# Kernel tuning notes

Hardware: AMD Instinct MI355X
Metric: run time of the kernel (lower is better)

Reference implementation:

```python
import jax, jax.numpy as jnp
import numpy as np

NUM_WIRES = 16
DEPTH = 3
BATCH = 128
DIM = 2 ** NUM_WIRES


def _apply_1q(psi, U, w, n):
    # Apply 2x2 gate U on wire w (wire 0 = most significant bit, PennyLane convention).
    B = psi.shape[0]
    psi = psi.reshape(B, 2 ** w, 2, -1)
    psi = jnp.einsum('ij,bpjq->bpiq', U, psi)
    return psi.reshape(B, -1)


def _apply_cnot(psi, c, t, n):
    # CNOT with control c, target t: flip target amplitudes where control bit is 1.
    B = psi.shape[0]
    a, b = min(c, t), max(c, t)
    psi = psi.reshape(B, 2 ** a, 2, 2 ** (b - a - 1), 2, 2 ** (n - b - 1))
    if c < t:
        psi = psi.at[:, :, 1].set(psi[:, :, 1, :, ::-1, :])
    else:
        psi = psi.at[:, :, :, :, 1].set(psi[:, :, ::-1, :, 1])
    return psi.reshape(B, -1)


def _pauli_z_signs(n):
    # signs[w, i] = +1 if bit w of basis state i is 0, else -1
    idx = np.arange(2 ** n)
    bits = (idx[None, :] >> (n - 1 - np.arange(n))[:, None]) & 1
    return jnp.asarray(1.0 - 2.0 * bits, dtype=jnp.float32)  # (n, 2^n)


def _circuit_features(state, params, n):
    psi = state.astype(jnp.complex64)  # (B, 2^n)
    depth = params.shape[0]
    half = params * 0.5
    for d in range(depth):
        for w in range(n):
            th, ph = half[d, w, 0], half[d, w, 1]
            cth, sth = jnp.cos(th), jnp.sin(th)
            em = jnp.exp(-1j * ph)   # RZ diag phase exp(-i*phi/2)
            ep = jnp.conj(em)
            # fused U = RZ(phi) @ RY(theta)
            U = jnp.stack([jnp.stack([em * cth, -em * sth]),
                           jnp.stack([ep * sth, ep * cth])])
            psi = _apply_1q(psi, U, w, n)
        for w in range(n - 1):
            psi = _apply_cnot(psi, w, w + 1, n)
        psi = _apply_cnot(psi, n - 1, 0, n)
    probs = psi.real ** 2 + psi.imag ** 2          # (B, 2^n)
    return probs @ _pauli_z_signs(n).T              # (B, n) PauliZ expvals


def setup_inputs() -> dict:
    key = jax.random.key(0)
    k1, k2, k3, k4 = jax.random.split(key, 4)
    state = jax.random.normal(k1, (BATCH, DIM), dtype=jnp.float32)
    state = state / jnp.linalg.norm(state, axis=1, keepdims=True)  # valid quantum state
    params = jax.random.normal(k2, (DEPTH, NUM_WIRES, 2), dtype=jnp.float32)
    head_w = jax.random.normal(k3, (1, NUM_WIRES), dtype=jnp.float32) / np.sqrt(NUM_WIRES)
    head_b = jax.random.normal(k4, (1,), dtype=jnp.float32)
    return {"state_batch": state, "params": params, "head_w": head_w, "head_b": head_b}


def reference(state_batch, params, head_w, head_b):
    feats = _circuit_features(state_batch, params, NUM_WIRES)  # (B, num_wires)
    return (feats @ head_w.T + head_b)[:, 0]                   # (B,)
```

## Files before the change

### kernel.cpp

```cpp
#include <hip/hip_runtime.h>
#include <hip/hip_fp16.h>

#define DIMQ 65536
#define BQ 128

typedef float v2f __attribute__((ext_vector_type(2)));

__host__ __device__ constexpr unsigned ring_map(unsigned x) {
  for (int bc = 15; bc >= 1; --bc) x ^= ((x >> bc) & 1u) << (bc - 1);
  x ^= (x & 1u) << 15;
  return x;
}
__host__ __device__ constexpr unsigned ring_unmap(unsigned y) {
  y ^= (y & 1u) << 15;
  for (int bc = 1; bc <= 15; ++bc) y ^= ((y >> bc) & 1u) << (bc - 1);
  return y;
}
__host__ __device__ constexpr unsigned row_of(int b) {
  return (b <= 14) ? ((0xFFFFu << b) & 0xFFFFu) : 0x7FFFu;
}
__host__ __device__ constexpr int popc16(unsigned v) {
  int c = 0; for (int i = 0; i < 16; ++i) c += (v >> i) & 1; return c;
}
static_assert(ring_unmap(ring_map(0x1234u)) == 0x1234u, "inv");
static_assert(ring_map(ring_unmap(0x5A5Au)) == 0x5A5Au, "inv");
__host__ __device__ constexpr bool check_rows() {
  const unsigned xs[4] = {0x1234u, 0x8001u, 0xFFFFu, 0x0F0Fu};
  for (int b = 0; b < 16; ++b)
    for (int i = 0; i < 4; ++i)
      if (((ring_map(xs[i]) >> b) & 1u) != (unsigned)(popc16(xs[i] & row_of(b)) & 1))
        return false;
  return true;
}
static_assert(check_rows(), "row_of = row b of M");
static_assert(ring_unmap(1u << 0)  == 0xC001u, "u0 = e0^e14^e15");
static_assert(ring_unmap(1u << 6)  == 0x0060u, "u6 = e5^e6");
static_assert(ring_unmap(1u << 11) == 0x0C00u, "u11 = e10^e11");
static_assert(ring_unmap(1u << 15) == 0xC000u, "u15 = e14^e15");
static_assert(ring_map(0x0C00u) == 0x0800u, "M(e10^e11)=e11");
static_assert(ring_map(0xC000u) == 0x8000u, "M(e14^e15)=e15");

__host__ __device__ constexpr unsigned loc13(unsigned z16) {
  return (z16 & 0x0FFFu) | (((z16 >> 15) & 1u) << 12);
}
__host__ __device__ constexpr unsigned sw13(unsigned i) { return i ^ ((i >> 5) & 31u); }

struct Tab32u { unsigned v[32]; };
__host__ __device__ constexpr Tab32u make_rx2() {
  Tab32u t{}; for (int r = 0; r < 32; ++r) t.v[r] = (unsigned)r << 11; return t;
}
__host__ __device__ constexpr Tab32u make_swrl() {
  Tab32u t{}; for (int r = 0; r < 32; ++r) t.v[r] = sw13(loc13(ring_map((unsigned)r)));
  return t;
}
__host__ __device__ constexpr Tab32u make_sw2() {
  Tab32u t{}; for (int r = 0; r < 32; ++r) t.v[r] = sw13((unsigned)r << 6);
  return t;
}
__host__ __device__ constexpr Tab32u make_rp3() {
  Tab32u t{}; for (int r = 0; r < 32; ++r) t.v[r] = (unsigned)r << 6; return t;
}
__host__ __device__ constexpr Tab32u make_t4() {
  Tab32u t{};
  for (int r = 0; r < 32; ++r) {
    unsigned r0 = r & 1, r1 = (r >> 1) & 1, r2 = (r >> 2) & 1, r3 = (r >> 3) & 1, r4 = (r >> 4) & 1;
    t.v[r] = (r0 << 10) | ((r0 ^ r1) << 11) | ((r1 ^ r2) << 12) |
             ((r2 ^ r3) << 13) | ((r3 ^ r4) << 14) | (r4 << 15);
  }
  return t;
}
__device__ constexpr Tab32u SWRL = make_swrl();
__device__ constexpr Tab32u SW2  = make_sw2();
__device__ constexpr Tab32u T4   = make_t4();

__host__ __device__ constexpr unsigned clmask(Tab32u t, unsigned row) {
  unsigned m = 0;
  for (int l = 0; l < 32; ++l)
    m |= (unsigned)(popc16(t.v[l] & row) & 1) << l;
  return m;
}
static_assert(clmask(make_t4(), 0xFFFFu) == 0u, "T4 chain has even parity");
static_assert(clmask(make_rx2(), row_of(1)) == 0x96696996u, "thue-morse parity of l");
static_assert((row_of(6) & 63u) == 0u && (row_of(14) & 63u) == 0u, "plain-sum bits");
static_assert((row_of(5) & 63u) == 32u && (row_of(4) & 63u) == 48u, "chain lo");
static_assert((row_of(3) & 63u) == 56u && (row_of(2) & 63u) == 60u, "chain mid");
static_assert((row_of(1) & 63u) == 62u && (row_of(0) & 63u) == 63u, "chain hi");
static_assert((row_of(15) & 63u) == 63u, "bit15 mask");
static_assert((row_of(0) & 31u) == 31u && (row_of(4) & 31u) == 16u, "suffix masks");
static_assert((row_of(5) & 31u) == 0u && (row_of(14) & 31u) == 0u, "rows 5..14 fixed");
static_assert((row_of(15) & 31u) == 31u, "row15 rides u0");
__host__ __device__ constexpr bool check_sufp() {
  for (unsigned r = 0; r < 32; ++r) {
    unsigned u = 0;
    for (int b = 0; b < 5; ++b) {
      unsigned s = 0; for (int j = b; j < 5; ++j) s ^= (r >> j) & 1;
      u |= s << b;
    }
    if ((u ^ (u >> 1)) != r) return false;
  }
  return true;
}
static_assert(check_sufp(), "suffix-parity inverse");

__global__ void k_prep(const float* __restrict__ params, float* __restrict__ uc) {
  int g = threadIdx.x;
  if (g >= 48) return;
  float th = 0.5f * params[g * 2 + 0];
  float ph = 0.5f * params[g * 2 + 1];
  float st, ct, sp, cp;
  __sincosf(th, &st, &ct);
  __sincosf(ph, &sp, &cp);
  float* u = uc + g * 8;
  u[0] = ct; u[1] = st;
  u[2] = cp; u[3] = -sp;
  u[4] = cp * cp - sp * sp;
  u[5] = 2.f * sp * cp;
  u[6] = 0.f; u[7] = 0.f;
}

struct CS { float ct, st; };
__device__ inline CS load_cs(const float* __restrict__ uc, int d, int w) {
  const float* u = uc + (d * 16 + w) * 8;
  return {u[0], u[1]};
}
__device__ inline v2f ldV(const float* __restrict__ uc, int d, int w) {
  const float* u = uc + (d * 16 + w) * 8;
  v2f r; r.x = u[2]; r.y = u[3]; return r;
}
__device__ inline v2f ldR(const float* __restrict__ uc, int d, int w) {
  const float* u = uc + (d * 16 + w) * 8;
  v2f r; r.x = u[4]; r.y = u[5]; return r;
}

__device__ inline v2f splat(float s) { v2f r; r.x = s; r.y = s; return r; }
__device__ inline v2f conjv(v2f a) { v2f r; r.x = a.x; r.y = -a.y; return r; }
__device__ inline v2f dsel(bool c, v2f v) { return c ? conjv(v) : v; }

__device__ inline v2f cmul(v2f c, v2f a) {
  v2f t;
  asm("v_pk_mul_f32 %0, %1, %2 op_sel:[0,0] op_sel_hi:[0,1]"
      : "=v"(t) : "v"(c), "v"(a));
  asm("v_pk_fma_f32 %0, %1, %2, %0 op_sel:[1,1,0] op_sel_hi:[1,0,1] neg_lo:[0,1,0]"
      : "+v"(t) : "v"(c), "v"(a));
  return t;
}
__device__ inline v2f cmulc(v2f c, v2f a) {
  v2f t;
  asm("v_pk_mul_f32 %0, %1, %2 op_sel:[0,0] op_sel_hi:[0,1]"
      : "=v"(t) : "v"(c), "v"(a));
  asm("v_pk_fma_f32 %0, %1, %2, %0 op_sel:[1,1,0] op_sel_hi:[1,0,1] neg_hi:[0,1,0]"
      : "+v"(t) : "v"(c), "v"(a));
  return t;
}

__device__ inline v2f h_to_f2(float bits) {
  __half2 h = __builtin_bit_cast(__half2, bits);
  float2 f = __half22float2(h);
  v2f r; r.x = f.x; r.y = f.y;
  return r;
}
__device__ inline float f2_to_h(v2f v) {
  __half2 h = __float22half2_rn(make_float2(v.x, v.y));
  return __builtin_bit_cast(float, h);
}

template <int MASK>
__device__ inline float lane_xor_f(float v) {
  if constexpr (MASK == 1) {
    return __int_as_float(__builtin_amdgcn_update_dpp(
        0, __float_as_int(v), 0xB1, 0xF, 0xF, true));
  } else if constexpr (MASK == 2) {
    return __int_as_float(__builtin_amdgcn_update_dpp(
        0, __float_as_int(v), 0x4E, 0xF, 0xF, true));
  } else if constexpr (MASK == 3) {
    return __int_as_float(__builtin_amdgcn_update_dpp(
        0, __float_as_int(v), 0x1B, 0xF, 0xF, true));
  } else if constexpr (MASK < 32) {
    return __int_as_float(__builtin_amdgcn_ds_swizzle(
        __float_as_int(v), (MASK << 10) | 0x1F));
  } else {
    return __shfl_xor(v, MASK, 64);
  }
}
template <int MASK>
__device__ inline v2f lane_xor_v(v2f v) {
  v2f r; r.x = lane_xor_f<MASK>(v.x); r.y = lane_xor_f<MASK>(v.y);
  return r;
}

__device__ inline void rmix2(v2f& o0, v2f CT, v2f S0_, v2f A0, v2f B0,
                             v2f& o1, v2f S1_, v2f A1, v2f B1) {
  v2f t0, t1;
  asm("v_pk_mul_f32 %0, %2, %3\n\t"
      "v_pk_mul_f32 %1, %5, %6\n\t"
      "v_pk_fma_f32 %0, %4, %7, %0\n\t"
      "v_pk_fma_f32 %1, %4, %8, %1"
      : "=&v"(t0), "=&v"(t1)
      : "v"(S0_), "v"(B0), "v"(CT), "v"(S1_), "v"(B1), "v"(A0), "v"(A1));
  o0 = t0; o1 = t1;
}

template <int K>
__device__ inline void reg_gate_r(v2f (&a)[32], CS u) {
  const v2f CT = splat(u.ct), SP = splat(u.st), SN = splat(-u.st);
#pragma unroll
  for (int l = 0; l < 32; ++l) {
    if (l & (1 << K)) continue;
    const int p = l | (1 << K);
    const v2f A = a[l], B = a[p];
    rmix2(a[l], CT, SN, A, B,
          a[p],     SP, B, A);
  }
}

template <int MASK>
__device__ inline void lane_gate_r(v2f (&a)[32], CS u, int lane) {
  const bool hi = (lane & MASK) != 0;
  const v2f CT = splat(u.ct), SS = splat(hi ? u.st : -u.st);
#pragma unroll
  for (int l = 0; l < 32; l += 2) {
    v2f p0 = lane_xor_v<MASK>(a[l]);
    v2f p1 = lane_xor_v<MASK>(a[l + 1]);
    rmix2(a[l],     CT, SS, a[l],     p0,
          a[l + 1],     SS, a[l + 1], p1);
  }
}

template <int MASK>
__device__ inline void lane_gate_sr(v2f (&a)[32], CS u, int hi) {
  const v2f CT = splat(u.ct), SS = splat(hi ? u.st : -u.st);
#pragma unroll
  for (int l = 0; l < 32; l += 2) {
    v2f p0 = lane_xor_v<MASK>(a[l]);
    v2f p1 = lane_xor_v<MASK>(a[l + 1]);
    rmix2(a[l],     CT, SS, a[l],     p0,
          a[l + 1],     SS, a[l + 1], p1);
  }
}

template <int PM, unsigned CLM>
__device__ inline void fused_reg_gate_r(v2f (&a)[32], CS u, unsigned xK,
                                        unsigned row) {
  const bool s = (__popc(xK & row) & 1) != 0;
  const v2f CT = splat(u.ct);
  const v2f S0 = splat(s ? u.st : -u.st), NS0 = splat(s ? -u.st : u.st);
  constexpr int LB = PM & (-PM);
#pragma unroll
  for (int l = 0; l < 32; ++l) {
    if (l & LB) continue;
    const int p = l ^ PM;
    const bool cl = (CLM >> l) & 1u;
    const v2f A = a[l], B = a[p];
    rmix2(a[l], CT, cl ? NS0 : S0, A, B,
          a[p],     cl ? S0 : NS0, B, A);
  }
}

template <int LM, unsigned CLM>
__device__ inline void fused_lane_gate_r(v2f (&a)[32], CS u, unsigned xK,
                                         unsigned row) {
  const bool s = (__popc(xK & row) & 1) != 0;
  const v2f CT = splat(u.ct);
  const v2f S0 = splat(s ? u.st : -u.st), NS0 = splat(s ? -u.st : u.st);
#pragma unroll
  for (int l = 0; l < 32; l += 2) {
    v2f p0 = lane_xor_v<LM>(a[l]);
    v2f p1 = lane_xor_v<LM>(a[l + 1]);
    const bool c0 = (CLM >> l) & 1u;
    const bool c1 = (CLM >> (l + 1)) & 1u;
    rmix2(a[l],     CT, c0 ? NS0 : S0, a[l],     p0,
          a[l + 1],     c1 ? NS0 : S0, a[l + 1], p1);
  }
}

template <int LM, int PM, unsigned CLM>
__device__ inline void fused_mixed_gate_r(v2f (&a)[32], CS u, unsigned xK,
                                          unsigned row) {
  const bool s = (__popc(xK & row) & 1) != 0;
  const v2f CT = splat(u.ct);
  const v2f S0 = splat(s ? u.st : -u.st), NS0 = splat(s ? -u.st : u.st);
  constexpr int LB = PM & (-PM);
#pragma unroll
  for (int l = 0; l < 32; ++l) {
    if (l & LB) continue;
    const int p = l ^ PM;
    const bool cl = (CLM >> l) & 1u;
    const bool cp = (CLM >> p) & 1u;
    const v2f A = a[l], B = a[p];
    v2f pa = lane_xor_v<LM>(B);
    v2f pb = lane_xor_v<LM>(A);
    rmix2(a[l], CT, cl ? NS0 : S0, A, pa,
          a[p],     cp ? NS0 : S0, B, pb);
  }
}

__device__ inline void apply_D0(v2f (&a)[32], const float* __restrict__ uc,
                                unsigned xK) {
  v2f c = dsel(xK & 1u, ldV(uc, 0, 15));
#pragma unroll
  for (int j = 1; j <= 10; ++j)
    c = cmul(dsel((xK >> j) & 1u, ldV(uc, 0, 15 - j)), c);
  v2f R[5];
#pragma unroll
  for (int k = 0; k < 5; ++k) {
    c = cmul(ldV(uc, 0, 4 - k), c);
    R[k] = ldR(uc, 0, 4 - k);
  }
  a[0] = cmul(c, a[0]);
#pragma unroll
  for (int i = 1; i < 32; ++i) {
    const int g = i ^ (i >> 1);
    const int k = __builtin_ctz((unsigned)i);
    const bool on = (g >> k) & 1;
    c = on ? cmul(R[k], c) : cmulc(R[k], c);
    a[g] = cmul(c, a[g]);
  }
}

__device__ inline void apply_D1(v2f (&a)[32], const float* __restrict__ uc,
                                unsigned xfull) {
  unsigned q = 0;
#pragma unroll
  for (int b = 0; b < 16; ++b)
    q |= (unsigned)(__popc(xfull & row_of(b)) & 1) << b;
  v2f c = dsel(q & 1u, ldV(uc, 1, 15));
#pragma unroll
  for (int b = 1; b < 16; ++b)
    c = cmul(dsel((q >> b) & 1u, ldV(uc, 1, 15 - b)), c);
  v2f RT[5];
#pragma unroll
  for (int b = 0; b < 5; ++b)
    RT[b] = dsel((q >> b) & 1u, ldR(uc, 1, 15 - b));
  RT[0] = cmul(dsel((q >> 15) & 1u, ldR(uc, 1, 0)), RT[0]);
  a[0] = cmul(c, a[0]);
#pragma unroll
  for (int i = 1; i < 32; ++i) {
    const int u = i ^ (i >> 1);
    const int k = __builtin_ctz((unsigned)i);
    const bool on = (u >> k) & 1;
    c = on ? cmul(RT[k], c) : cmulc(RT[k], c);
    const int r = u ^ (u >> 1);
    a[r] = cmul(c, a[r]);
  }
}

__global__ __launch_bounds__(256, 4)
void k_p1(const float* __restrict__ in, __half2* __restrict__ dstb,
          const float* __restrict__ uc) {
  const int b = blockIdx.x >> 3;
  const unsigned hi = blockIdx.x & 7;
  const unsigned wg = threadIdx.x >> 6;
  const unsigned lane = threadIdx.x & 63;
  const unsigned xK = (hi << 13) | (wg << 11) | (lane << 2);
  const float* src = in + (size_t)b * DIMQ;
  v2f a[32];
#pragma unroll
  for (int c = 0; c < 8; ++c) {
    float4 q = *(const float4*)(src + xK + ((unsigned)c << 8));
    a[c * 4 + 0].x = q.x; a[c * 4 + 0].y = 0.f;
    a[c * 4 + 1].x = q.y; a[c * 4 + 1].y = 0.f;
    a[c * 4 + 2].x = q.z; a[c * 4 + 2].y = 0.f;
    a[c * 4 + 3].x = q.w; a[c * 4 + 3].y = 0.f;
  }
  reg_gate_r<0>(a, load_cs(uc, 0, 15));
  reg_gate_r<1>(a, load_cs(uc, 0, 14));
  lane_gate_r<1 >(a, load_cs(uc, 0, 13), lane);
  lane_gate_r<2 >(a, load_cs(uc, 0, 12), lane);
  lane_gate_r<4 >(a, load_cs(uc, 0, 11), lane);
  lane_gate_r<8 >(a, load_cs(uc, 0, 10), lane);
  lane_gate_r<16>(a, load_cs(uc, 0, 9 ), lane);
  lane_gate_r<32>(a, load_cs(uc, 0, 8 ), lane);
  reg_gate_r<2>(a, load_cs(uc, 0, 7));
  reg_gate_r<3>(a, load_cs(uc, 0, 6));
  reg_gate_r<4>(a, load_cs(uc, 0, 5));
  float* dst = (float*)(dstb + (size_t)b * DIMQ);
#pragma unroll
  for (int c = 0; c < 8; ++c) {
    float4 q;
    q.x = f2_to_h(a[c * 4 + 0]);
    q.y = f2_to_h(a[c * 4 + 1]);
    q.z = f2_to_h(a[c * 4 + 2]);
    q.w = f2_to_h(a[c * 4 + 3]);
    *(float4*)(dst + xK + ((unsigned)c << 8)) = q;
  }
}

__global__ __launch_bounds__(256, 4)
void k_p2(const __half2* __restrict__ srcb, __half2* __restrict__ dstb,
          const float* __restrict__ uc) {
  const int b = blockIdx.x >> 3;
  const unsigned t8 = blockIdx.x & 7;
  const unsigned wg = threadIdx.x >> 6;
  const unsigned lane = threadIdx.x & 63;
  const unsigned xK = (t8 << 8) | (wg << 6) | lane;
  const float* src = (const float*)(srcb + (size_t)b * DIMQ);
  float* dst = (float*)(dstb + (size_t)b * DIMQ);
  v2f a[32];
#pragma unroll
  for (int r = 0; r < 32; ++r)
    a[r] = h_to_f2(src[((unsigned)r << 11) | xK]);
  reg_gate_r<0>(a, load_cs(uc, 0, 4));
  reg_gate_r<1>(a, load_cs(uc, 0, 3));
  reg_gate_r<2>(a, load_cs(uc, 0, 2));
  reg_gate_r<3>(a, load_cs(uc, 0, 1));
  reg_gate_r<4>(a, load_cs(uc, 0, 0));
  apply_D0(a, uc, xK);
  fused_lane_gate_r<3 , clmask(make_rx2(), row_of(1))>(a, load_cs(uc, 1, 14), xK, row_of(1));
  fused_lane_gate_r<6 , clmask(make_rx2(), row_of(2))>(a, load_cs(uc, 1, 13), xK, row_of(2));
  fused_lane_gate_r<12, clmask(make_rx2(), row_of(3))>(a, load_cs(uc, 1, 12), xK, row_of(3));
  fused_lane_gate_r<24, clmask(make_rx2(), row_of(4))>(a, load_cs(uc, 1, 11), xK, row_of(4));
  fused_lane_gate_r<48, clmask(make_rx2(), row_of(5))>(a, load_cs(uc, 1, 10), xK, row_of(5));
  fused_mixed_gate_r<1, 0x18, clmask(make_rx2(), 0xFFFFu)>(a, load_cs(uc, 1, 15), xK, 0xFFFFu);
  fused_reg_gate_r<3 , clmask(make_rx2(), row_of(12))>(a, load_cs(uc, 1, 3), xK, row_of(12));
  fused_reg_gate_r<6 , clmask(make_rx2(), row_of(13))>(a, load_cs(uc, 1, 2), xK, row_of(13));
  fused_reg_gate_r<12, clmask(make_rx2(), row_of(14))>(a, load_cs(uc, 1, 1), xK, row_of(14));
  fused_reg_gate_r<24, clmask(make_rx2(), row_of(15))>(a, load_cs(uc, 1, 0), xK, row_of(15));
#pragma unroll
  for (int r = 0; r < 32; ++r)
    dst[((unsigned)r << 11) | xK] = f2_to_h(a[r]);
}

__global__ __launch_bounds__(256, 3)
void k_p3(const __half2* __restrict__ srcb, __half2* __restrict__ dstb,
          const float* __restrict__ uc) {
  __shared__ float lds[8192];
  const int b = blockIdx.x >> 3;
  const unsigned tb = blockIdx.x & 7;
  const unsigned x12 = tb & 1u, x13 = (tb >> 1) & 1u, tt = tb >> 2;
  const unsigned tid = threadIdx.x;
  const float* src = (const float*)(srcb + (size_t)b * DIMQ);
  float* dst = (float*)(dstb + (size_t)b * DIMQ);
#pragma unroll
  for (unsigned c = 0; c < 2; ++c) {
    const unsigned gbase = (c << 14) | ((c ^ tt) << 15) | (x13 << 13) | (x12 << 12);
#pragma unroll
    for (unsigned j = 0; j < 4; ++j) {
      const unsigned e = j * 1024u + tid * 4u;
      float4 q = *(const float4*)(src + gbase + e);
      const unsigned idx = (c << 12) | e;
      const unsigned m = (idx >> 5) & 31u;
      if (m & 1u) { float s0 = q.x; q.x = q.y; q.y = s0; s0 = q.z; q.z = q.w; q.w = s0; }
      if (m & 2u) { float s0 = q.x, s1 = q.y; q.x = q.z; q.y = q.w; q.z = s0; q.w = s1; }
      *(float4*)&lds[(idx ^ m) & ~3u] = q;
    }
  }
  __syncthreads();
  const unsigned lane = tid & 63u, wv = tid >> 6;
  const unsigned w0 = wv & 1u, w1 = wv >> 1;
  const unsigned g = (lane ^ (lane >> 1)) & 63u;
  const unsigned x5 = (lane ^ w0) & 1u;
  const unsigned xloc  = (x5 << 5) | (g << 6) | (w1 << 12);
  const unsigned xfull = (x5 << 5) | (g << 6) | (x12 << 12) | (x13 << 13)
                       | (w1 << 14) | ((w1 ^ tt) << 15);
  const unsigned sb1 = sw13(xloc);
  v2f a[32];
#pragma unroll
  for (unsigned r = 0; r < 32; ++r) a[r] = h_to_f2(lds[sb1 ^ r]);
  lane_gate_sr<1 >(a, load_cs(uc, 1, 9), __popc(xfull & row_of(6 )) & 1);
  lane_gate_sr<2 >(a, load_cs(uc, 1, 8), __popc(xfull & row_of(7 )) & 1);
  lane_gate_sr<4 >(a, load_cs(uc, 1, 7), __popc(xfull & row_of(8 )) & 1);
  lane_gate_sr<8 >(a, load_cs(uc, 1, 6), __popc(xfull & row_of(9 )) & 1);
  lane_gate_sr<16>(a, load_cs(uc, 1, 5), __popc(xfull & row_of(10)) & 1);
  lane_gate_sr<32>(a, load_cs(uc, 1, 4), __popc(xfull & row_of(11)) & 1);
  apply_D1(a, uc, xfull);
  const unsigned swzr = sw13(loc13(ring_map(xfull)));
  __syncthreads();
#pragma unroll
  for (unsigned r = 0; r < 32; ++r) lds[swzr ^ SWRL.v[r]] = f2_to_h(a[r]);
  __syncthreads();
  const unsigned z12 = x12 ^ x13 ^ tt, z13 = x13 ^ tt, z14 = tt;
  const unsigned zloc2 = lane | (w0 << 11) | (w1 << 12);
  const unsigned sb2 = sw13(zloc2);
  const unsigned z16b = lane | (w0 << 11) | (z12 << 12) | (z13 << 13)
                      | (z14 << 14) | (w1 << 15);
#pragma unroll
  for (unsigned r = 0; r < 32; ++r) a[r] = h_to_f2(lds[sb2 ^ SW2.v[r]]);
  fused_lane_gate_r<3 , clmask(make_rp3(), row_of(1))>(a, load_cs(uc, 2, 14), z16b, row_of(1));
  fused_lane_gate_r<6 , clmask(make_rp3(), row_of(2))>(a, load_cs(uc, 2, 13), z16b, row_of(2));
  fused_lane_gate_r<12, clmask(make_rp3(), row_of(3))>(a, load_cs(uc, 2, 12), z16b, row_of(3));
  fused_lane_gate_r<24, clmask(make_rp3(), row_of(4))>(a, load_cs(uc, 2, 11), z16b, row_of(4));
  fused_lane_gate_r<48, clmask(make_rp3(), row_of(5))>(a, load_cs(uc, 2, 10), z16b, row_of(5));
  fused_mixed_gate_r<32, 1, clmask(make_rp3(), row_of(6))>(a, load_cs(uc, 2, 9), z16b, row_of(6));
  fused_reg_gate_r<3 , clmask(make_rp3(), row_of(7 ))>(a, load_cs(uc, 2, 8), z16b, row_of(7));
  fused_reg_gate_r<6 , clmask(make_rp3(), row_of(8 ))>(a, load_cs(uc, 2, 7), z16b, row_of(8));
  fused_reg_gate_r<12, clmask(make_rp3(), row_of(9 ))>(a, load_cs(uc, 2, 6), z16b, row_of(9));
  fused_reg_gate_r<24, clmask(make_rp3(), row_of(10))>(a, load_cs(uc, 2, 5), z16b, row_of(10));
#pragma unroll
  for (unsigned r = 0; r < 32; ++r)
    dst[z16b ^ (r << 6)] = f2_to_h(a[r]);
}

__device__ inline float rsum6(float s) {
  s += __shfl_xor(s, 1, 64);  s += __shfl_xor(s, 2, 64);
  s += __shfl_xor(s, 4, 64);  s += __shfl_xor(s, 8, 64);
  s += __shfl_xor(s, 16, 64); s += __shfl_xor(s, 32, 64);
  return s;
}
template <int NB>
__device__ inline float rsum_lo(float s) {
  if constexpr (NB >= 1) s += __shfl_xor(s, 1, 64);
  if constexpr (NB >= 2) s += __shfl_xor(s, 2, 64);
  if constexpr (NB >= 3) s += __shfl_xor(s, 4, 64);
  if constexpr (NB >= 4) s += __shfl_xor(s, 8, 64);
  if constexpr (NB >= 5) s += __shfl_xor(s, 16, 64);
  return s;
}

__global__ __launch_bounds__(256, 4)
void k_p4(const __half2* __restrict__ srcb, float* __restrict__ partials,
          const float* __restrict__ uc) {
  const int b = blockIdx.x >> 3;
  const unsigned q = blockIdx.x & 7;
  const unsigned wg = threadIdx.x >> 6, lane = threadIdx.x & 63u;
  const unsigned zb = lane | ((wg & 1u) << 6) | ((wg >> 1) << 7) | ((q & 1u) << 8)
                    | (((q >> 1) & 1u) << 9) | ((q >> 2) << 10);
  const float* src = (const float*)(srcb + (size_t)b * DIMQ);
  v2f a[32];
#pragma unroll
  for (unsigned r = 0; r < 32; ++r) a[r] = h_to_f2(src[zb ^ T4.v[r]]);
  fused_reg_gate_r<1 , clmask(make_t4(), row_of(11))>(a, load_cs(uc, 2, 4), zb, row_of(11));
  fused_reg_gate_r<2 , clmask(make_t4(), row_of(12))>(a, load_cs(uc, 2, 3), zb, row_of(12));
  fused_reg_gate_r<4 , clmask(make_t4(), row_of(13))>(a, load_cs(uc, 2, 2), zb, row_of(13));
  fused_reg_gate_r<8 , clmask(make_t4(), row_of(14))>(a, load_cs(uc, 2, 1), zb, row_of(14));
  fused_reg_gate_r<16, clmask(make_t4(), row_of(15))>(a, load_cs(uc, 2, 0), zb, row_of(15));
  fused_mixed_gate_r<1, 16, clmask(make_t4(), 0xFFFFu)>(a, load_cs(uc, 2, 15), zb, 0xFFFFu);
  float s_tot = 0.f, s_b0 = 0.f, s_b1 = 0.f, s_b2 = 0.f, s_b3 = 0.f, s_b4 = 0.f;
#pragma unroll
  for (unsigned r = 0; r < 32; ++r) {
    const float p = fmaf(a[r].x, a[r].x, a[r].y * a[r].y);
    s_tot += p;
    s_b0 += (r & 1u)  ? -p : p;
    s_b1 += (r & 2u)  ? -p : p;
    s_b2 += (r & 4u)  ? -p : p;
    s_b3 += (r & 8u)  ? -p : p;
    s_b4 += (r & 16u) ? -p : p;
  }
  const float Rtot = rsum6(s_tot);
  const float Rb0 = rsum6(s_b0);
  const float Rb1 = rsum6(s_b1);
  const float Rb2 = rsum6(s_b2);
  const float Rb3 = rsum6(s_b3);
  const float c5      = s_tot  - __shfl_xor(s_tot,  32, 64);
  const float c45     = c5     - __shfl_xor(c5,     16, 64);
  const float c345    = c45    - __shfl_xor(c45,     8, 64);
  const float c2345   = c345   - __shfl_xor(c345,    4, 64);
  const float c12345  = c2345  - __shfl_xor(c2345,   2, 64);
  const float c012345 = c12345 - __shfl_xor(c12345,  1, 64);
  const float F32 = rsum_lo<5>(c5);
  const float F48 = rsum_lo<4>(c45);
  const float F56 = rsum_lo<3>(c345);
  const float F60 = rsum_lo<2>(c2345);
  const float F62 = rsum_lo<1>(c12345);
  const float F63t = c012345;
  float d = s_b4;
  d -= __shfl_xor(d, 32, 64); d -= __shfl_xor(d, 16, 64);
  d -= __shfl_xor(d,  8, 64); d -= __shfl_xor(d,  4, 64);
  d -= __shfl_xor(d,  2, 64); d -= __shfl_xor(d,  1, 64);
  const float F63b4 = d;
  if (lane == 0) {
    const unsigned ybh = ring_map(zb & ~63u);
    const float V[16] = {F63b4, Rb3, Rb2, Rb1, Rb0,
                         Rtot, Rtot, Rtot, Rtot, Rtot,
                         F32, F48, F56, F60, F62, F63t};
    const unsigned t = q * 4 + wg;
    float* dstp = partials + ((size_t)b * 32 + t) * 16;
#pragma unroll
    for (int w = 0; w < 16; ++w) {
      const int bit = 15 - w;
      dstp[w] = ((ybh >> bit) & 1u) ? -V[w] : V[w];
    }
  }
}

__global__ __launch_bounds__(256)
void k_head(const float* __restrict__ partials, const float* __restrict__ hw,
            const float* __restrict__ hb, float* __restrict__ out) {
  const int b = blockIdx.x;
  const int t = threadIdx.x;
  const int w = t & 15;
  const int i = t >> 4;
  float s = partials[((size_t)b * 32 + i) * 16 + w] +
            partials[((size_t)b * 32 + i + 16) * 16 + w];
  __shared__ float red[256];
  __shared__ float feats[16];
  red[t] = s;
  __syncthreads();
  if (t < 16) {
    float f = 0.f;
    for (int j = 0; j < 16; ++j) f += red[j * 16 + t];
    feats[t] = f;
  }
  __syncthreads();
  if (t == 0) {
    float o = hb[0];
    for (int w2 = 0; w2 < 16; ++w2) o = fmaf(feats[w2], hw[w2], o);
    out[b] = o;
  }
}

extern "C" void kernel_launch(void* const* d_in, const int* in_sizes, int n_in,
                              void* d_out, int out_size, void* d_ws, size_t ws_size,
                              hipStream_t stream) {
  const float* state  = (const float*)d_in[0];
  const float* params = (const float*)d_in[1];
  const float* head_w = (const float*)d_in[2];
  const float* head_b = (const float*)d_in[3];
  float* out = (float*)d_out;

  __half2* bufA = (__half2*)d_ws;
  __half2* bufB = bufA + (size_t)DIMQ * BQ;
  __half2* bufC = bufB + (size_t)DIMQ * BQ;
  float*   partials = (float*)(bufC + (size_t)DIMQ * BQ);
  float*   uc = partials + (size_t)BQ * 32 * 16;

  k_prep<<<dim3(1), dim3(64), 0, stream>>>(params, uc);

  const dim3 g(1024), blk(256);
  k_p1<<<g, blk, 0, stream>>>(state, bufA, uc);
  k_p2<<<g, blk, 0, stream>>>(bufA, bufB, uc);
  k_p3<<<g, blk, 0, stream>>>(bufB, bufC, uc);
  k_p4<<<g, blk, 0, stream>>>(bufC, partials, uc);
  k_head<<<dim3(128), blk, 0, stream>>>(partials, head_w, head_b, out);
}
```

Measured before the change: 154.0 us.

## Keep real-valued state packed as real pairs through first layer RY gates

The first layer's RY rotations keep the state real, so the kernels now pack two real amplitudes per v2f instead of one complex with a zero imaginary part. This halves the register count and arithmetic for those gates, and the intermediate buffer between the first two kernels is stored as real fp16 instead of complex half2, halving that memory traffic. The RZ phase diagonal then expands the packed reals back to complex values. The risk is narrower per-element loads in k_p2 (scalar half loads), which may coalesce less well.

```diff
diff --git a/kernel.cpp b/kernel.cpp
--- a/kernel.cpp
+++ b/kernel.cpp
@@ -152,6 +152,17 @@
       : "+v"(t) : "v"(c), "v"(a));
   return t;
 }
+template <int H>
+__device__ inline v2f cmulr(v2f c, v2f pk) {
+  v2f t;
+  if constexpr (H == 0)
+    asm("v_pk_mul_f32 %0, %1, %2 op_sel:[0,0] op_sel_hi:[1,0]"
+        : "=v"(t) : "v"(c), "v"(pk));
+  else
+    asm("v_pk_mul_f32 %0, %1, %2 op_sel:[0,1] op_sel_hi:[1,1]"
+        : "=v"(t) : "v"(c), "v"(pk));
+  return t;
+}
 
 __device__ inline v2f h_to_f2(float bits) {
   __half2 h = __builtin_bit_cast(__half2, bits);
@@ -200,11 +211,29 @@
   o0 = t0; o1 = t1;
 }
 
+__device__ inline void pswap2(v2f& r0, v2f CT, v2f S, v2f A0, v2f& r1, v2f A1) {
+  v2f t0, t1;
+  asm("v_pk_mul_f32 %0, %2, %4 op_sel:[0,1] op_sel_hi:[1,0] neg_lo:[0,1]\n\t"
+      "v_pk_mul_f32 %1, %2, %5 op_sel:[0,1] op_sel_hi:[1,0] neg_lo:[0,1]\n\t"
+      "v_pk_fma_f32 %0, %3, %4, %0\n\t"
+      "v_pk_fma_f32 %1, %3, %5, %1"
+      : "=&v"(t0), "=&v"(t1)
+      : "v"(S), "v"(CT), "v"(A0), "v"(A1));
+  r0 = t0; r1 = t1;
+}
+
+__device__ inline void packed_gate16(v2f (&a)[16], CS u) {
+  const v2f CT = splat(u.ct), S = splat(u.st);
+#pragma unroll
+  for (int l = 0; l < 16; l += 2)
+    pswap2(a[l], CT, S, a[l], a[l + 1], a[l + 1]);
+}
+
 template <int K>
-__device__ inline void reg_gate_r(v2f (&a)[32], CS u) {
+__device__ inline void pr_gate16(v2f (&a)[16], CS u) {
   const v2f CT = splat(u.ct), SP = splat(u.st), SN = splat(-u.st);
 #pragma unroll
-  for (int l = 0; l < 32; ++l) {
+  for (int l = 0; l < 16; ++l) {
     if (l & (1 << K)) continue;
     const int p = l | (1 << K);
     const v2f A = a[l], B = a[p];
@@ -214,11 +243,11 @@
 }
 
 template <int MASK>
-__device__ inline void lane_gate_r(v2f (&a)[32], CS u, int lane) {
+__device__ inline void lane_gate16(v2f (&a)[16], CS u, int lane) {
   const bool hi = (lane & MASK) != 0;
   const v2f CT = splat(u.ct), SS = splat(hi ? u.st : -u.st);
 #pragma unroll
-  for (int l = 0; l < 32; l += 2) {
+  for (int l = 0; l < 16; l += 2) {
     v2f p0 = lane_xor_v<MASK>(a[l]);
     v2f p1 = lane_xor_v<MASK>(a[l + 1]);
     rmix2(a[l],     CT, SS, a[l],     p0,
@@ -294,8 +323,8 @@
   }
 }
 
-__device__ inline void apply_D0(v2f (&a)[32], const float* __restrict__ uc,
-                                unsigned xK) {
+__device__ inline void apply_D0p(const v2f (&pk)[16], v2f (&a)[32],
+                                 const float* __restrict__ uc, unsigned xK) {
   v2f c = dsel(xK & 1u, ldV(uc, 0, 15));
 #pragma unroll
   for (int j = 1; j <= 10; ++j)
@@ -306,14 +335,14 @@
     c = cmul(ldV(uc, 0, 4 - k), c);
     R[k] = ldR(uc, 0, 4 - k);
   }
-  a[0] = cmul(c, a[0]);
+  a[0] = cmulr<0>(c, pk[0]);
 #pragma unroll
   for (int i = 1; i < 32; ++i) {
     const int g = i ^ (i >> 1);
     const int k = __builtin_ctz((unsigned)i);
     const bool on = (g >> k) & 1;
     c = on ? cmul(R[k], c) : cmulc(R[k], c);
-    a[g] = cmul(c, a[g]);
+    a[g] = (g & 1) ? cmulr<1>(c, pk[g >> 1]) : cmulr<0>(c, pk[g >> 1]);
   }
 }
 
@@ -345,7 +374,7 @@
 }
 
 __global__ __launch_bounds__(256, 4)
-void k_p1(const float* __restrict__ in, __half2* __restrict__ dstb,
+void k_p1(const float* __restrict__ in, __half* __restrict__ dstb,
           const float* __restrict__ uc) {
   const int b = blockIdx.x >> 3;
   const unsigned hi = blockIdx.x & 7;
@@ -353,58 +382,57 @@
   const unsigned lane = threadIdx.x & 63;
   const unsigned xK = (hi << 13) | (wg << 11) | (lane << 2);
   const float* src = in + (size_t)b * DIMQ;
-  v2f a[32];
+  v2f a[16];
 #pragma unroll
   for (int c = 0; c < 8; ++c) {
     float4 q = *(const float4*)(src + xK + ((unsigned)c << 8));
-    a[c * 4 + 0].x = q.x; a[c * 4 + 0].y = 0.f;
-    a[c * 4 + 1].x = q.y; a[c * 4 + 1].y = 0.f;
-    a[c * 4 + 2].x = q.z; a[c * 4 + 2].y = 0.f;
-    a[c * 4 + 3].x = q.w; a[c * 4 + 3].y = 0.f;
-  }
-  reg_gate_r<0>(a, load_cs(uc, 0, 15));
-  reg_gate_r<1>(a, load_cs(uc, 0, 14));
-  lane_gate_r<1 >(a, load_cs(uc, 0, 13), lane);
-  lane_gate_r<2 >(a, load_cs(uc, 0, 12), lane);
-  lane_gate_r<4 >(a, load_cs(uc, 0, 11), lane);
-  lane_gate_r<8 >(a, load_cs(uc, 0, 10), lane);
-  lane_gate_r<16>(a, load_cs(uc, 0, 9 ), lane);
-  lane_gate_r<32>(a, load_cs(uc, 0, 8 ), lane);
-  reg_gate_r<2>(a, load_cs(uc, 0, 7));
-  reg_gate_r<3>(a, load_cs(uc, 0, 6));
-  reg_gate_r<4>(a, load_cs(uc, 0, 5));
-  float* dst = (float*)(dstb + (size_t)b * DIMQ);
+    a[c * 2 + 0].x = q.x; a[c * 2 + 0].y = q.y;
+    a[c * 2 + 1].x = q.z; a[c * 2 + 1].y = q.w;
+  }
+  packed_gate16(a, load_cs(uc, 0, 15));
+  pr_gate16<0>(a, load_cs(uc, 0, 14));
+  lane_gate16<1 >(a, load_cs(uc, 0, 13), lane);
+  lane_gate16<2 >(a, load_cs(uc, 0, 12), lane);
+  lane_gate16<4 >(a, load_cs(uc, 0, 11), lane);
+  lane_gate16<8 >(a, load_cs(uc, 0, 10), lane);
+  lane_gate16<16>(a, load_cs(uc, 0, 9 ), lane);
+  lane_gate16<32>(a, load_cs(uc, 0, 8 ), lane);
+  pr_gate16<1>(a, load_cs(uc, 0, 7));
+  pr_gate16<2>(a, load_cs(uc, 0, 6));
+  pr_gate16<3>(a, load_cs(uc, 0, 5));
+  __half* dst = dstb + (size_t)b * DIMQ;
 #pragma unroll
   for (int c = 0; c < 8; ++c) {
-    float4 q;
-    q.x = f2_to_h(a[c * 4 + 0]);
-    q.y = f2_to_h(a[c * 4 + 1]);
-    q.z = f2_to_h(a[c * 4 + 2]);
-    q.w = f2_to_h(a[c * 4 + 3]);
-    *(float4*)(dst + xK + ((unsigned)c << 8)) = q;
+    float2 w;
+    w.x = f2_to_h(a[c * 2 + 0]);
+    w.y = f2_to_h(a[c * 2 + 1]);
+    *(float2*)(dst + xK + ((unsigned)c << 8)) = w;
   }
 }
 
 __global__ __launch_bounds__(256, 4)
-void k_p2(const __half2* __restrict__ srcb, __half2* __restrict__ dstb,
+void k_p2(const __half* __restrict__ srcb, __half2* __restrict__ dstb,
           const float* __restrict__ uc) {
   const int b = blockIdx.x >> 3;
   const unsigned t8 = blockIdx.x & 7;
   const unsigned wg = threadIdx.x >> 6;
   const unsigned lane = threadIdx.x & 63;
   const unsigned xK = (t8 << 8) | (wg << 6) | lane;
-  const float* src = (const float*)(srcb + (size_t)b * DIMQ);
+  const __half* src = srcb + (size_t)b * DIMQ;
   float* dst = (float*)(dstb + (size_t)b * DIMQ);
+  v2f pk[16];
+#pragma unroll
+  for (int k = 0; k < 16; ++k) {
+    pk[k].x = __half2float(src[((unsigned)(2 * k) << 11) | xK]);
+    pk[k].y = __half2float(src[((unsigned)(2 * k + 1) << 11) | xK]);
+  }
+  packed_gate16(pk, load_cs(uc, 0, 4));
+  pr_gate16<0>(pk, load_cs(uc, 0, 3));
+  pr_gate16<1>(pk, load_cs(uc, 0, 2));
+  pr_gate16<2>(pk, load_cs(uc, 0, 1));
+  pr_gate16<3>(pk, load_cs(uc, 0, 0));
   v2f a[32];
-#pragma unroll
-  for (int r = 0; r < 32; ++r)
-    a[r] = h_to_f2(src[((unsigned)r << 11) | xK]);
-  reg_gate_r<0>(a, load_cs(uc, 0, 4));
-  reg_gate_r<1>(a, load_cs(uc, 0, 3));
-  reg_gate_r<2>(a, load_cs(uc, 0, 2));
-  reg_gate_r<3>(a, load_cs(uc, 0, 1));
-  reg_gate_r<4>(a, load_cs(uc, 0, 0));
-  apply_D0(a, uc, xK);
+  apply_D0p(pk, a, uc, xK);
   fused_lane_gate_r<3 , clmask(make_rx2(), row_of(1))>(a, load_cs(uc, 1, 14), xK, row_of(1));
   fused_lane_gate_r<6 , clmask(make_rx2(), row_of(2))>(a, load_cs(uc, 1, 13), xK, row_of(2));
   fused_lane_gate_r<12, clmask(make_rx2(), row_of(3))>(a, load_cs(uc, 1, 12), xK, row_of(3));
@@ -607,8 +635,8 @@
   const float* head_b = (const float*)d_in[3];
   float* out = (float*)d_out;
 
-  __half2* bufA = (__half2*)d_ws;
-  __half2* bufB = bufA + (size_t)DIMQ * BQ;
+  __half*  bufA = (__half*)d_ws;
+  __half2* bufB = (__half2*)(bufA + (size_t)DIMQ * BQ);
   __half2* bufC = bufB + (size_t)DIMQ * BQ;
   float*   partials = (float*)(bufC + (size_t)DIMQ * BQ);
   float*   uc = partials + (size_t)BQ * 32 * 16;
```

New measurement: 147.7 us. -4.1%, faster.
